# Kernel tuning notes

Hardware: AMD Instinct MI355X
Metric: run time of the kernel (lower is better)

## Reference

```python
import jax, jax.numpy as jnp
import numpy as np

POS_THR = 0.5      # ROI_POSITIVE_THR
NEG_THR = 0.1      # ROI_NEGATIVE_THR
N_SAMPLES = 256    # ROI_SAMPLES
FG_RATIO = 0.25    # ROI_SAMPLE_RATIO
L1W = 1.0          # RPN.L1WEIGHT_INTERSECTION
NUM_FG = int(N_SAMPLES * FG_RATIO)


def _make_boxes(kxy, kwh, shape):
    # valid [x1,y1,x2,y2] boxes in an ~800px image
    xy = jax.random.uniform(kxy, shape[:-1] + (2,)) * 800.0
    wh = jax.random.uniform(kwh, shape[:-1] + (2,)) * 200.0 + 1.0
    return jnp.concatenate([xy, xy + wh], axis=-1)


def setup_inputs() -> dict:
    key = jax.random.key(0)
    k1, k2, k3, k4 = jax.random.split(key, 4)
    proposals = _make_boxes(k1, k2, (16, 16384, 4))  # [B, N, 4]
    gt_boxes = _make_boxes(k3, k4, (16, 128, 4))     # [B, G, 4]
    return {"proposals": proposals, "gt_boxes": gt_boxes}


def _centrehw(b):
    # [x1,y1,x2,y2] -> [cx,cy,w,h]
    x1, y1, x2, y2 = b[..., 0], b[..., 1], b[..., 2], b[..., 3]
    return jnp.stack([(x1 + x2) * 0.5, (y1 + y2) * 0.5, x2 - x1, y2 - y1], axis=-1)


def _targets(gt_c, roi_c):
    dx = (gt_c[..., 0] - roi_c[..., 0]) / roi_c[..., 2]
    dy = (gt_c[..., 1] - roi_c[..., 1]) / roi_c[..., 3]
    dw = jnp.log(gt_c[..., 2] / roi_c[..., 2])
    dh = jnp.log(gt_c[..., 3] / roi_c[..., 3])
    return jnp.stack([dx, dy, dw, dh], axis=-1)


def _iou(prop, gt):
    # prop [B,N,4], gt [B,G,4] -> IoU [B,N,G]
    p = prop[:, :, None, :]
    g = gt[:, None, :, :]
    ix1 = jnp.maximum(p[..., 0], g[..., 0])
    iy1 = jnp.maximum(p[..., 1], g[..., 1])
    ix2 = jnp.minimum(p[..., 2], g[..., 2])
    iy2 = jnp.minimum(p[..., 3], g[..., 3])
    inter = jnp.clip(ix2 - ix1, 0.0) * jnp.clip(iy2 - iy1, 0.0)
    ap = (p[..., 2] - p[..., 0]) * (p[..., 3] - p[..., 1])
    ag = (g[..., 2] - g[..., 0]) * (g[..., 3] - g[..., 1])
    return inter / jnp.maximum(ap + ag - inter, 1e-8)


def _forward(proposals, gt_boxes):
    B, N, _ = proposals.shape
    iou = _iou(proposals, gt_boxes)                       # [B,N,G]
    max_iou = iou.max(axis=-1)                            # [B,N]
    argmax_gt = iou.argmax(axis=-1).astype(jnp.int32)     # [B,N]
    # classify: 1=fg, 0=bg, -1=ignore
    labels = jnp.where(max_iou >= POS_THR, 1,
                       jnp.where(max_iou < NEG_THR, 0, -1)).astype(jnp.int32)
    # randsample: keep <= NUM_FG positives (random), fill rest with negatives.
    r = jax.random.uniform(jax.random.key(1), (B, N))
    pos = labels == 1
    r_pos = jnp.where(pos, r, -1.0)
    order = jnp.argsort(-r_pos, axis=1)
    ranks = jnp.argsort(order, axis=1)                    # rank among positives by r
    pos_sel = pos & (ranks < NUM_FG)
    prio = jnp.where(pos_sel, 3.0 + r,
                     jnp.where(labels == 0, 2.0 + r,
                               jnp.where(pos, 1.0 + r, r)))
    _, idx = jax.lax.top_k(prio, N_SAMPLES)               # [B,S] sampled proposal ids
    batch_labels = jnp.maximum(jnp.take_along_axis(labels, idx, axis=1), 0)  # [B,S]
    roi_batch = jnp.take_along_axis(proposals, idx[..., None], axis=1)       # [B,S,4]
    sel_gt = jnp.take_along_axis(argmax_gt, idx, axis=1)                     # [B,S]
    gt_batch = jnp.take_along_axis(gt_boxes, sel_gt[..., None], axis=1)      # [B,S,4]
    bbox_targets = _targets(_centrehw(gt_batch), _centrehw(roi_batch))       # [B,S,4]
    in_w = jnp.where((batch_labels == 1)[..., None], L1W, 0.0)
    in_w = jnp.broadcast_to(in_w, bbox_targets.shape)
    out_w = (in_w > 0).astype(jnp.float32)
    return roi_batch, batch_labels, bbox_targets, in_w, out_w


def reference(proposals, gt_boxes):
    return _forward(proposals, gt_boxes)
```

## Files before the change

kernel.cpp:

```cpp
#include <hip/hip_runtime.h>
#include <stdint.h>

#define BATCH 16
#define NPROP 16384
#define NGT   128
#define NSAMP 256
#define NFG   64
#define GCAP  512

__device__ __forceinline__ void thr_block(uint32_t c0, uint32_t c1,
                                          uint32_t* o0, uint32_t* o1) {
    const uint32_t k0 = 0u, k1 = 1u, ks2 = 0x1BD11BDBu;
    uint32_t x0 = c0 + k0, x1 = c1 + k1;
#define RND(d) { x0 += x1; x1 = (x1 << d) | (x1 >> (32 - d)); x1 ^= x0; }
    RND(13) RND(15) RND(26) RND(6)   x0 += k1;  x1 += ks2 + 1u;
    RND(17) RND(29) RND(16) RND(24)  x0 += ks2; x1 += k0 + 2u;
    RND(13) RND(15) RND(26) RND(6)   x0 += k0;  x1 += k1 + 3u;
    RND(17) RND(29) RND(16) RND(24)  x0 += k1;  x1 += ks2 + 4u;
    RND(13) RND(15) RND(26) RND(6)   x0 += ks2; x1 += k0 + 5u;
#undef RND
    *o0 = x0; *o1 = x1;
}

__device__ __forceinline__ uint32_t thr_part_xor(uint32_t f) {
    uint32_t a, b; thr_block(0u, f, &a, &b);
    return a ^ b;
}

__global__ void __launch_bounds__(256) k_compute(
    const float* __restrict__ props, const float* __restrict__ gts,
    uint32_t* __restrict__ packed)
{
#pragma clang fp contract(off)
    const int b = blockIdx.y;
    const int n = blockIdx.x * 256 + threadIdx.x;
    __shared__ float4 g4[NGT];
    if (threadIdx.x < NGT)
        g4[threadIdx.x] = ((const float4*)gts)[(size_t)b * NGT + threadIdx.x];
    __syncthreads();
    const float4 pb = ((const float4*)props)[(size_t)b * NPROP + n];
    const float ap = (pb.z - pb.x) * (pb.w - pb.y);
    float best = -1.0f; int bg = 0;
    #pragma unroll 4
    for (int i = 0; i < NGT; ++i) {
        const float4 gb = g4[i];
        float ag = (gb.z - gb.x) * (gb.w - gb.y);
        float w = fmaxf(fminf(pb.z, gb.z) - fmaxf(pb.x, gb.x), 0.0f);
        float h = fmaxf(fminf(pb.w, gb.w) - fmaxf(pb.y, gb.y), 0.0f);
        float inter = w * h;
        float un = fmaxf(ap + ag - inter, 1e-8f);
        float iou = inter / un;
        if (iou > best) { best = iou; bg = i; }
    }
    uint32_t lab = (best >= 0.5f) ? 2u : ((best < 0.1f) ? 1u : 0u);
    const uint32_t f = (uint32_t)b * NPROP + (uint32_t)n;
    packed[f] = ((thr_part_xor(f) >> 9) << 9) | (lab << 7) | (uint32_t)bg;
}

__device__ __forceinline__ float r_from_packed(uint32_t p) {
    return __uint_as_float(0x3F800000u | (p >> 9)) - 1.0f;
}

__device__ __forceinline__ uint64_t keyA(uint32_t p, uint32_t n) {
    return (((uint64_t)(p >> 9)) << 14) | (uint64_t)(16383u - n);
}
__device__ __forceinline__ uint64_t keyB(uint32_t p, uint32_t n, uint64_t thrA) {
    uint32_t lab = (p >> 7) & 3u;
    float r = r_from_packed(p);
    float prio;
    if (lab == 2u)      prio = (keyA(p, n) >= thrA) ? (3.0f + r) : (1.0f + r);
    else if (lab == 1u) prio = 2.0f + r;
    else                prio = r;
    return (((uint64_t)__float_as_uint(prio)) << 14) | (uint64_t)(16383u - n);
}

__global__ void __launch_bounds__(1024) k_select(
    const float* __restrict__ props, const float* __restrict__ gts,
    const uint32_t* __restrict__ packed, float* __restrict__ out)
{
#pragma clang fp contract(off)
    const int b = blockIdx.x;
    const int tid = threadIdx.x;
    __shared__ uint32_t spk[NPROP];
    __shared__ uint32_t hist[2048];
    __shared__ uint64_t gat[GCAP];
    __shared__ uint32_t sh_npos, sel_cnt, gcnt;
    __shared__ uint32_t sh_dig, sh_k, sh_cnt_in;
    __shared__ uint64_t sh_thr;
    __shared__ uint64_t sel_keys[NSAMP];

    const uint32_t* pk = packed + (size_t)b * NPROP;
    if (tid == 0) { sh_npos = 0; sel_cnt = 0; }
    __syncthreads();
    {
        uint32_t c = 0;
        for (int i = 0; i < 16; i++) {
            uint32_t p = pk[tid + i * 1024];
            spk[tid + i * 1024] = p;
            c += (((p >> 7) & 3u) == 2u);
        }
        #pragma unroll
        for (int off = 32; off > 0; off >>= 1) c += __shfl_down(c, off);
        if ((tid & 63) == 0) atomicAdd(&sh_npos, c);
    }
    __syncthreads();
    const uint32_t npos = sh_npos;

    uint64_t thrA = 0, thrB = 0;
    for (int phase = (npos > NFG ? 0 : 1); phase < 2; ++phase) {
        uint32_t k = (phase == 0) ? NFG : NSAMP;
        int shift = (phase == 0) ? 26 : 34;
        uint64_t prefix = 0, mask = 0;
        for (;;) {
            hist[tid] = 0; hist[tid + 1024] = 0;
            __syncthreads();
            for (int i = 0; i < 16; i++) {
                uint32_t n = (uint32_t)(tid + i * 1024);
                uint32_t p = spk[n];
                bool elig; uint64_t key;
                if (phase == 0) { elig = (((p >> 7) & 3u) == 2u); key = keyA(p, n); }
                else            { elig = true;                     key = keyB(p, n, thrA); }
                if (elig && ((key ^ prefix) & mask) == 0)
                    atomicAdd(&hist[(uint32_t)(key >> shift) & 2047u], 1u);
            }
            __syncthreads();
            if (tid < 64) {
                const uint32_t lane = tid;
                uint32_t cs = 0;
                if (lane < 32) {
                    const int base = (int)lane * 64;
                    #pragma unroll 8
                    for (int i = 0; i < 64; i++) cs += hist[base + i];
                }
                uint32_t s = cs;
                #pragma unroll
                for (int off = 1; off < 32; off <<= 1) {
                    uint32_t t = __shfl_down(s, off);
                    if (lane + off < 32) s += t;
                }
                uint32_t sExcl = s - cs;
                bool cond = (lane < 32) && (sExcl < k) && (k <= s);
                uint64_t ball = __ballot(cond);
                uint32_t cstar = (uint32_t)(__ffsll((unsigned long long)ball) - 1);
                uint32_t kc = __shfl(k - sExcl, (int)cstar);
                uint32_t val = hist[cstar * 64 + lane];
                uint32_t fi = val;
                #pragma unroll
                for (int off = 1; off < 64; off <<= 1) {
                    uint32_t t = __shfl_down(fi, off);
                    if (lane + off < 64) fi += t;
                }
                uint32_t fExcl = fi - val;
                bool cond2 = (fExcl < kc) && (kc <= fi);
                uint64_t ball2 = __ballot(cond2);
                uint32_t bstar = (uint32_t)(__ffsll((unsigned long long)ball2) - 1);
                if (lane == bstar) {
                    sh_dig = cstar * 64 + lane;
                    sh_k = kc - fExcl;
                    sh_cnt_in = val;
                }
            }
            __syncthreads();
            uint32_t dig = sh_dig, kk = sh_k, cnt = sh_cnt_in;
            prefix |= ((uint64_t)dig) << shift;
            mask   |= 2047ull << shift;
            if (cnt <= GCAP || shift == 0) {
                if (tid == 0) gcnt = 0;
                __syncthreads();
                for (int i = 0; i < 16; i++) {
                    uint32_t n = (uint32_t)(tid + i * 1024);
                    uint32_t p = spk[n];
                    bool elig; uint64_t key;
                    if (phase == 0) { elig = (((p >> 7) & 3u) == 2u); key = keyA(p, n); }
                    else            { elig = true;                     key = keyB(p, n, thrA); }
                    if (elig && ((key ^ prefix) & mask) == 0) {
                        uint32_t s = atomicAdd(&gcnt, 1u);
                        if (s < GCAP) gat[s] = key;
                    }
                }
                __syncthreads();
                uint32_t gc = (gcnt < GCAP) ? gcnt : GCAP;
                if (tid < gc) {
                    uint64_t x = gat[tid];
                    uint32_t r = 0;
                    for (uint32_t j = 0; j < gc; j++) r += (gat[j] > x);
                    if (r == kk - 1) sh_thr = x;
                }
                __syncthreads();
                break;
            } else {
                k = kk;
                shift = (shift >= 11) ? shift - 11 : 0;
                __syncthreads();
            }
        }
        if (phase == 0) thrA = sh_thr; else thrB = sh_thr;
        __syncthreads();
    }

    for (int i = 0; i < 16; i++) {
        uint32_t n = (uint32_t)(tid + i * 1024);
        uint64_t key = keyB(spk[n], n, thrA);
        if (key >= thrB) {
            uint32_t slot = atomicAdd(&sel_cnt, 1u);
            if (slot < NSAMP) sel_keys[slot] = key;
        }
    }
    __syncthreads();

    if (tid < NSAMP) {
        uint64_t x = sel_keys[tid];
        uint32_t r = 0;
        for (int j = 0; j < NSAMP; j++) r += (sel_keys[j] > x);
        uint32_t n = 16383u - (uint32_t)(x & 0x3FFFu);
        uint32_t p = spk[n];
        uint32_t lab = (p >> 7) & 3u;
        uint32_t bg = p & 0x7Fu;
        const float4 pb = ((const float4*)props)[(size_t)b * NPROP + n];
        const float4 gb = ((const float4*)gts)[(size_t)b * NGT + bg];
        const size_t O_ROI = 0;
        const size_t O_LBL = (size_t)BATCH * NSAMP * 4;
        const size_t O_TGT = O_LBL + (size_t)BATCH * NSAMP;
        const size_t O_INW = O_TGT + (size_t)BATCH * NSAMP * 4;
        const size_t O_OUW = O_INW + (size_t)BATCH * NSAMP * 4;
        const size_t row = (size_t)b * NSAMP + r;
        out[O_ROI + row * 4 + 0] = pb.x;
        out[O_ROI + row * 4 + 1] = pb.y;
        out[O_ROI + row * 4 + 2] = pb.z;
        out[O_ROI + row * 4 + 3] = pb.w;
        const int isfg = (lab == 2u) ? 1 : 0;
        out[O_LBL + row] = isfg ? 1.0f : 0.0f;
        float rw  = pb.z - pb.x, rh = pb.w - pb.y;
        float gw  = gb.z - gb.x, gh = gb.w - gb.y;
        out[O_TGT + row * 4 + 0] = ((gb.x + gb.z) * 0.5f - (pb.x + pb.z) * 0.5f) / rw;
        out[O_TGT + row * 4 + 1] = ((gb.y + gb.w) * 0.5f - (pb.y + pb.w) * 0.5f) / rh;
        out[O_TGT + row * 4 + 2] = logf(gw / rw);
        out[O_TGT + row * 4 + 3] = logf(gh / rh);
        float wv = isfg ? 1.0f : 0.0f;
        for (int c = 0; c < 4; c++) {
            out[O_INW + row * 4 + c] = wv;
            out[O_OUW + row * 4 + c] = wv;
        }
    }
}

extern "C" void kernel_launch(void* const* d_in, const int* in_sizes, int n_in,
                              void* d_out, int out_size, void* d_ws, size_t ws_size,
                              hipStream_t stream) {
    (void)in_sizes; (void)n_in; (void)out_size; (void)ws_size;
    const float* props = (const float*)d_in[0];
    const float* gts   = (const float*)d_in[1];
    uint32_t* packed = (uint32_t*)d_ws;
    float* out = (float*)d_out;

    dim3 gridA(NPROP / 256, BATCH);
    k_compute<<<gridA, 256, 0, stream>>>(props, gts, packed);
    k_select<<<BATCH, 1024, 0, stream>>>(props, gts, packed, out);
}
```

Before: 113.1 us.

## Restrict phase-2 radix select to the boundary priority class and vectorize loads

Counts positives and negatives up front, works out which priority class (selected-fg, bg, unselected-fg, ignore) holds the 256th sample, and runs the phase-2 radix select only over elements of that class with a reduced k. The starting shift is adjusted per class, so the top-level histogram pass can skip the bits shared by the class exponent. The initial global-to-shared copy now uses uint4 vector loads. The aim is fewer radix passes and less atomic contention, at the cost of extra class computation per element and more complex threshold logic.

Result: faster. 108.0 us (-4.6%).

```diff
diff --git a/kernel.cpp b/kernel.cpp
--- a/kernel.cpp
+++ b/kernel.cpp
@@ -64,13 +64,14 @@
 __device__ __forceinline__ uint64_t keyA(uint32_t p, uint32_t n) {
     return (((uint64_t)(p >> 9)) << 14) | (uint64_t)(16383u - n);
 }
+__device__ __forceinline__ uint32_t cls_of(uint32_t p, uint32_t n, uint64_t thrA) {
+    uint32_t lab = (p >> 7) & 3u;
+    if (lab == 2u) return (keyA(p, n) >= thrA) ? 3u : 1u;
+    return (lab == 1u) ? 2u : 0u;
+}
 __device__ __forceinline__ uint64_t keyB(uint32_t p, uint32_t n, uint64_t thrA) {
-    uint32_t lab = (p >> 7) & 3u;
     float r = r_from_packed(p);
-    float prio;
-    if (lab == 2u)      prio = (keyA(p, n) >= thrA) ? (3.0f + r) : (1.0f + r);
-    else if (lab == 1u) prio = 2.0f + r;
-    else                prio = r;
+    float prio = (float)cls_of(p, n, thrA) + r;
     return (((uint64_t)__float_as_uint(prio)) << 14) | (uint64_t)(16383u - n);
 }
 
@@ -81,35 +82,51 @@
 #pragma clang fp contract(off)
     const int b = blockIdx.x;
     const int tid = threadIdx.x;
-    __shared__ uint32_t spk[NPROP];
+    __shared__ uint4 spk4[NPROP / 4];
     __shared__ uint32_t hist[2048];
     __shared__ uint64_t gat[GCAP];
-    __shared__ uint32_t sh_npos, sel_cnt, gcnt;
+    __shared__ uint32_t sh_pos, sh_neg, sel_cnt, gcnt;
     __shared__ uint32_t sh_dig, sh_k, sh_cnt_in;
     __shared__ uint64_t sh_thr;
     __shared__ uint64_t sel_keys[NSAMP];
-
-    const uint32_t* pk = packed + (size_t)b * NPROP;
-    if (tid == 0) { sh_npos = 0; sel_cnt = 0; }
+    uint32_t* spk = (uint32_t*)spk4;
+
+    const uint4* pk4 = (const uint4*)(packed + (size_t)b * NPROP);
+    if (tid == 0) { sh_pos = 0; sh_neg = 0; sel_cnt = 0; }
     __syncthreads();
     {
-        uint32_t c = 0;
-        for (int i = 0; i < 16; i++) {
-            uint32_t p = pk[tid + i * 1024];
-            spk[tid + i * 1024] = p;
-            c += (((p >> 7) & 3u) == 2u);
-        }
+        uint32_t cp = 0, cn = 0;
         #pragma unroll
-        for (int off = 32; off > 0; off >>= 1) c += __shfl_down(c, off);
-        if ((tid & 63) == 0) atomicAdd(&sh_npos, c);
-    }
-    __syncthreads();
-    const uint32_t npos = sh_npos;
+        for (int i = 0; i < 4; i++) {
+            uint4 v = pk4[tid + i * 1024];
+            spk4[tid + i * 1024] = v;
+            cp += (((v.x >> 7) & 3u) == 2u) + (((v.y >> 7) & 3u) == 2u)
+                + (((v.z >> 7) & 3u) == 2u) + (((v.w >> 7) & 3u) == 2u);
+            cn += (((v.x >> 7) & 3u) == 1u) + (((v.y >> 7) & 3u) == 1u)
+                + (((v.z >> 7) & 3u) == 1u) + (((v.w >> 7) & 3u) == 1u);
+        }
+        #pragma unroll
+        for (int off = 32; off > 0; off >>= 1) {
+            cp += __shfl_down(cp, off);
+            cn += __shfl_down(cn, off);
+        }
+        if ((tid & 63) == 0) { atomicAdd(&sh_pos, cp); atomicAdd(&sh_neg, cn); }
+    }
+    __syncthreads();
+    const uint32_t npos = sh_pos;
+    const uint32_t c3 = (npos < NFG) ? npos : NFG;
+    const uint32_t c2 = sh_neg;
+    const uint32_t c1 = npos - c3;
 
     uint64_t thrA = 0, thrB = 0;
     for (int phase = (npos > NFG ? 0 : 1); phase < 2; ++phase) {
-        uint32_t k = (phase == 0) ? NFG : NSAMP;
-        int shift = (phase == 0) ? 26 : 34;
+        uint32_t k; int shift; uint32_t clsStar = 0;
+        if (phase == 0) { k = NFG; shift = 26; }
+        else {
+            if (NSAMP <= c3 + c2)           { clsStar = 2; k = NSAMP - c3;           shift = 25; }
+            else if (NSAMP <= c3 + c2 + c1) { clsStar = 1; k = NSAMP - c3 - c2;      shift = 26; }
+            else                            { clsStar = 0; k = NSAMP - c3 - c2 - c1; shift = 34; }
+        }
         uint64_t prefix = 0, mask = 0;
         for (;;) {
             hist[tid] = 0; hist[tid + 1024] = 0;
@@ -119,7 +136,7 @@
                 uint32_t p = spk[n];
                 bool elig; uint64_t key;
                 if (phase == 0) { elig = (((p >> 7) & 3u) == 2u); key = keyA(p, n); }
-                else            { elig = true;                     key = keyB(p, n, thrA); }
+                else { elig = (cls_of(p, n, thrA) == clsStar); key = keyB(p, n, thrA); }
                 if (elig && ((key ^ prefix) & mask) == 0)
                     atomicAdd(&hist[(uint32_t)(key >> shift) & 2047u], 1u);
             }
@@ -172,7 +189,7 @@
                     uint32_t p = spk[n];
                     bool elig; uint64_t key;
                     if (phase == 0) { elig = (((p >> 7) & 3u) == 2u); key = keyA(p, n); }
-                    else            { elig = true;                     key = keyB(p, n, thrA); }
+                    else { elig = (cls_of(p, n, thrA) == clsStar); key = keyB(p, n, thrA); }
                     if (elig && ((key ^ prefix) & mask) == 0) {
                         uint32_t s = atomicAdd(&gcnt, 1u);
                         if (s < GCAP) gat[s] = key;
```
